# Kernel optimization log

Measured on AMD Instinct MI355X. Metric: run time of the kernel, lower is better.

## Reference

```python
import jax, jax.numpy as jnp
import numpy as np

# Bit-slice quantization config (MSB-first; first 1-bit slice is the sign slice)
INPUT_SLICE = (1, 2, 2, 2)    # 7 bits total
WEIGHT_SLICE = (1, 2, 2, 2)   # 7 bits total
INPUT_GRAN = 32               # input quant granularity along K (per unfolded row)
WEIGHT_GRAN_K = 32            # weight quant granularity along K
WEIGHT_GRAN_N = 32            # weight quant granularity along N
STRIDE = 1
PAD = 1
KSIZE = 3


def _quantize(x, max_abs, total_bits):
    """Symmetric per-granule quantization to signed total_bits integers."""
    max_val = float((1 << (total_bits - 1)) - 1)
    scale = max_abs / max_val
    scale = jnp.where(scale == 0, jnp.ones_like(scale), scale)
    q = jnp.clip(jnp.round(x / scale), -max_val, max_val)
    return q, scale


def _slice_recombine(q, slice_bits):
    """Emulate the bit-slice path: decompose signed int q (two's complement)
    into slices per slice_bits (MSB first), then recombine exactly as the
    crossbar MapReduce accumulation 'sum_i slice_i * 2^offset_i' would."""
    t = int(sum(slice_bits))
    qi = q.astype(jnp.int32)
    u = jnp.where(qi < 0, qi + (1 << t), qi)  # two's complement unsigned rep
    recomb = jnp.zeros_like(u)
    off = t
    for b in slice_bits:  # fixed, small slice loop
        off -= b
        s = (u >> off) & ((1 << b) - 1)
        recomb = recomb + (s << off)
    recomb = jnp.where(recomb >= (1 << (t - 1)), recomb - (1 << t), recomb)
    return recomb.astype(jnp.float32)


def _fake_quant_input(x):
    # x: (B, L, K) unfolded activations; granularity (1, INPUT_GRAN)
    B, L, K = x.shape
    g = INPUT_GRAN
    xg = x.reshape(B, L, K // g, g)
    max_abs = jnp.max(jnp.abs(xg), axis=-1, keepdims=True)
    q, scale = _quantize(xg, max_abs, sum(INPUT_SLICE))
    q = _slice_recombine(q, INPUT_SLICE)
    deq = (q * scale).reshape(B, L, K)
    # straight-through estimator (matches custom autograd conv2d_mem_func)
    return x + jax.lax.stop_gradient(deq - x)


def _fake_quant_weight(w):
    # w: (K, N) reshaped weight; granularity (WEIGHT_GRAN_K, WEIGHT_GRAN_N)
    K, N = w.shape
    gk, gn = WEIGHT_GRAN_K, WEIGHT_GRAN_N
    wg = w.reshape(K // gk, gk, N // gn, gn)
    max_abs = jnp.max(jnp.abs(wg), axis=(1, 3), keepdims=True)
    q, scale = _quantize(wg, max_abs, sum(WEIGHT_SLICE))
    q = _slice_recombine(q, WEIGHT_SLICE)
    deq = (q * scale).reshape(K, N)
    return w + jax.lax.stop_gradient(deq - w)


def _unfold(x, k, stride, pad):
    # torch.F.unfold semantics -> (B, L, C*k*k), C-major ordering
    B, C, H, W = x.shape
    xp = jnp.pad(x, ((0, 0), (0, 0), (pad, pad), (pad, pad)))
    Ho = (H + 2 * pad - k) // stride + 1
    Wo = (W + 2 * pad - k) // stride + 1
    cols = []
    for ki in range(k):  # fixed small kernel loop
        for kj in range(k):
            cols.append(xp[:, :, ki:ki + stride * Ho:stride, kj:kj + stride * Wo:stride])
    patches = jnp.stack(cols, axis=2)              # (B, C, k*k, Ho, Wo)
    patches = patches.reshape(B, C * k * k, Ho * Wo)
    return patches.transpose(0, 2, 1), Ho, Wo      # (B, L, K)


def setup_inputs() -> dict:
    key = jax.random.key(0)
    k1, k2, k3 = jax.random.split(key, 3)
    B, C, H, W = 8, 256, 56, 56
    N = 256
    fan_in = C * KSIZE * KSIZE
    x = jax.random.normal(k1, (B, C, H, W), dtype=jnp.float32)
    weight = jax.random.normal(k2, (N, C, KSIZE, KSIZE), dtype=jnp.float32) / np.sqrt(fan_in)
    bias = jax.random.normal(k3, (N,), dtype=jnp.float32) / np.sqrt(fan_in)
    return {"input": x, "weight": weight, "bias": bias}


def reference(input, weight, bias):
    B = input.shape[0]
    N = weight.shape[0]
    cols, Ho, Wo = _unfold(input, KSIZE, STRIDE, PAD)     # (B, L, K)
    w2d = weight.reshape(N, -1).T                         # (K, N)
    xq = _fake_quant_input(cols)
    wq = _fake_quant_weight(w2d)
    out = jnp.einsum('blk,kn->bln', xq, wq) + bias        # (B, L, N)
    out = out.transpose(0, 2, 1).reshape(B, N, Ho, Wo)    # fold with 1x1 kernel
    return out
```

## Files before the change

### kernel.cpp

```cpp
#include <hip/hip_runtime.h>
#include <hip/hip_bf16.h>
#include <stdint.h>

#define KD 2304
#define LD 3136
#define ND 256
#define MD 25088
#define CD 256
#define PITCH 64
#define PROWS 58
#define PLANE (PROWS * PITCH)

typedef __bf16 bf16x8 __attribute__((ext_vector_type(8)));
typedef float f32x4 __attribute__((ext_vector_type(4)));
typedef float f32x4u __attribute__((ext_vector_type(4), aligned(4)));

__device__ __forceinline__ void gload_lds16(const void* g, void* l) {
  __builtin_amdgcn_global_load_lds(
      (const __attribute__((address_space(1))) unsigned int*)g,
      (__attribute__((address_space(3))) unsigned int*)l, 16, 0, 0);
}

__global__ __launch_bounds__(256) void prep_kernel(
    const float* __restrict__ x, float* __restrict__ xpad,
    const float* __restrict__ w, __hip_bfloat16* __restrict__ wqT) {
  if (blockIdx.x < 2048) {
    const int plane = blockIdx.x;
    const float* src = x + (size_t)plane * LD;
    float* dst = xpad + (size_t)plane * PLANE;
    const int cc4 = (threadIdx.x & 15) * 4;
    const int r0 = threadIdx.x >> 4;
#pragma unroll
    for (int p = 0; p < 4; ++p) {
      const int r = r0 + p * 16;
      if (r >= PROWS) continue;
      f32x4 o = {0.f, 0.f, 0.f, 0.f};
      if (r >= 1 && r <= 56) {
        const float* srow = src + (r - 1) * 56;
        if (cc4 == 0) {
          f32x4u v = *(const f32x4u*)(srow);
          o[1] = v[0]; o[2] = v[1]; o[3] = v[2];
        } else if (cc4 <= 52) {
          o = *(const f32x4u*)(srow + cc4 - 1);
        } else if (cc4 == 56) {
          f32x4u v = *(const f32x4u*)(srow + 52);
          o[0] = v[3];
        }
      }
      *(f32x4*)(dst + r * PITCH + cc4) = o;
    }
  } else {
    const int wb = blockIdx.x - 2048;
    const int gk = wb % 72;
    const int gn = wb / 72;
    const int n = gn * 32 + (threadIdx.x >> 3);
    const int k = gk * 32 + (threadIdx.x & 7) * 4;
    const float4 v = *(const float4*)(w + (size_t)n * KD + k);
    float a = fmaxf(fmaxf(fabsf(v.x), fabsf(v.y)), fmaxf(fabsf(v.z), fabsf(v.w)));
#pragma unroll
    for (int m = 1; m <= 32; m <<= 1) a = fmaxf(a, __shfl_xor(a, m, 64));
    __shared__ float red[4];
    if ((threadIdx.x & 63) == 0) red[threadIdx.x >> 6] = a;
    __syncthreads();
    const float mx = fmaxf(fmaxf(red[0], red[1]), fmaxf(red[2], red[3]));
    const float r63 = (mx == 0.f) ? 0.f : 63.f / mx;
    const float scale = mx * (1.f / 63.f);
    ushort4 o;
    o.x = __builtin_bit_cast(unsigned short, __float2bfloat16(rintf(v.x * r63) * scale));
    o.y = __builtin_bit_cast(unsigned short, __float2bfloat16(rintf(v.y * r63) * scale));
    o.z = __builtin_bit_cast(unsigned short, __float2bfloat16(rintf(v.z * r63) * scale));
    o.w = __builtin_bit_cast(unsigned short, __float2bfloat16(rintf(v.w * r63) * scale));
    *(ushort4*)((unsigned short*)wqT + (size_t)n * KD + k) = o;
  }
}

__device__ __forceinline__ void qload_u(const float* __restrict__ pb, int p0,
                                        int c0, f32x4u (&win)[5][3]) {
#pragma unroll
  for (int dc = 0; dc < 5; ++dc) {
    const int cdc = (c0 + dc > 255) ? 255 : c0 + dc;
    const float* cp = pb + p0 + cdc * PLANE;
#pragma unroll
    for (int di = 0; di < 3; ++di)
      win[dc][di] = *(const f32x4u*)(cp + di * PITCH);
  }
}

template <int KP0>
__device__ __forceinline__ void qfinishT(const f32x4u (&win)[5][3],
                                         char* __restrict__ as_base,
                                         int lane, unsigned cbase) {
  float v[32];
#pragma unroll
  for (int t = 0; t < 32; ++t) {
    const int idx = KP0 + t;
    v[t] = win[idx / 9][(idx % 9) / 3][(idx % 9) % 3];
  }
  float m16[16];
#pragma unroll
  for (int t = 0; t < 16; ++t)
    m16[t] = fmaxf(__builtin_fabsf(v[2 * t]), __builtin_fabsf(v[2 * t + 1]));
#pragma unroll
  for (int t = 0; t < 8; ++t) m16[t] = fmaxf(m16[t], m16[t + 8]);
#pragma unroll
  for (int t = 0; t < 4; ++t) m16[t] = fmaxf(m16[t], m16[t + 4]);
  const float mx = fmaxf(fmaxf(m16[0], m16[1]), fmaxf(m16[2], m16[3]));
  float r63 = 63.f * __builtin_amdgcn_rcpf(mx);
  r63 = (mx == 0.f) ? 0.f : r63;
  const float scale = mx * (1.f / 63.f);
  unsigned pk[16];
#pragma unroll
  for (int t = 0; t < 16; ++t) {
    const float a = rintf(v[2 * t] * r63) * scale;
    const float b = rintf(v[2 * t + 1] * r63) * scale;
    unsigned d;
    asm("v_cvt_pk_bf16_f32 %0, %1, %2" : "=v"(d) : "v"(a), "v"(b));
    pk[t] = d;
  }
  char* row = as_base + lane * 128;
  const unsigned swz = (unsigned)((lane & 7) << 4);
#pragma unroll
  for (int s = 0; s < 4; ++s) {
    uint4 o = {pk[4 * s], pk[4 * s + 1], pk[4 * s + 2], pk[4 * s + 3]};
    *(uint4*)(row + ((cbase + (unsigned)(s * 16)) ^ swz)) = o;
  }
}

#define SW_FIN(PH, DST, CB)                                                   \
  switch (PH) {                                                               \
    case 0: qfinishT<0>(win, DST, lane, CB); break;                           \
    case 1: qfinishT<1>(win, DST, lane, CB); break;                           \
    case 2: qfinishT<2>(win, DST, lane, CB); break;                           \
    case 3: qfinishT<3>(win, DST, lane, CB); break;                           \
    case 4: qfinishT<4>(win, DST, lane, CB); break;                           \
    case 5: qfinishT<5>(win, DST, lane, CB); break;                           \
    case 6: qfinishT<6>(win, DST, lane, CB); break;                           \
    case 7: qfinishT<7>(win, DST, lane, CB); break;                           \
    default: qfinishT<8>(win, DST, lane, CB); break;                          \
  }

__device__ __forceinline__ void stage_ns(const unsigned short* __restrict__ wsrc,
                                         int k0, int lane, int w,
                                         char* __restrict__ NsH) {
#pragma unroll
  for (int sg = 0; sg < 8; ++sg) {
    const int c = w * 8 + sg;
    const int row = c * 8 + (lane >> 3);
    const int u = (lane & 7) ^ (row & 7);
    gload_lds16(wsrc + (size_t)row * KD + k0 + u * 8, NsH + c * 1024 + lane * 16);
  }
}

__device__ __forceinline__ void mfma_phase(
    const char* __restrict__ As0, const char* __restrict__ As1,
    const char* __restrict__ Ns0, const char* __restrict__ Ns1,
    f32x4 (&acc)[4][4], int w, int lq, int hv) {
#pragma unroll
  for (int kk = 0; kk < 4; ++kk) {
    const char* NsH = (kk < 2) ? Ns0 : Ns1;
    const char* AsH = (kk < 2) ? As0 : As1;
    const int kl = kk & 1;
    bf16x8 af[4], bf[4];
#pragma unroll
    for (int i = 0; i < 4; ++i) {
      const unsigned rn = (unsigned)(w * 64 + i * 16 + lq);
      const unsigned u = (unsigned)((kl * 4 + hv) ^ (rn & 7));
      af[i] = *(const bf16x8*)(NsH + rn * 128u + u * 16u);
    }
#pragma unroll
    for (int j = 0; j < 4; ++j) {
      const unsigned rm = (unsigned)(j * 16 + lq);
      const unsigned u = (unsigned)((kl * 4 + hv) ^ (rm & 7));
      bf[j] = *(const bf16x8*)(AsH + rm * 128u + u * 16u);
    }
#pragma unroll
    for (int i = 0; i < 4; ++i)
#pragma unroll
      for (int j = 0; j < 4; ++j)
        acc[i][j] = __builtin_amdgcn_mfma_f32_16x16x32_bf16(
            af[i], bf[j], acc[i][j], 0, 0, 0);
  }
}

__global__ __launch_bounds__(256, 2) void fused_gemm_kernel(
    const float* __restrict__ xpad, const __hip_bfloat16* __restrict__ wqT,
    const float* __restrict__ bias, float* __restrict__ out) {
  extern __shared__ char smem[];
  char* As0 = smem;
  char* As1 = smem + 8192;
  char* Ns0 = smem + 16384;
  char* Ns1 = smem + 49152;
  const int tid = threadIdx.x;
  const int lane = tid & 63;
  const int w = __builtin_amdgcn_readfirstlane(tid >> 6);

  const int bid = blockIdx.x;
  const int mt = (bid & 7) * 49 + (bid >> 3);
  const int m0 = mt * 64;

  const int b = m0 / LD;
  const int l = m0 - b * LD + lane;
  const int i = l / 56;
  const int j = l - i * 56;
  const float* pb = xpad + (size_t)b * CD * PLANE;
  const int p0 = i * PITCH + j;
  const unsigned short* wsrc = (const unsigned short*)wqT;

  char* as_dst = (w < 2) ? As0 : As1;
  const unsigned cb = (unsigned)((w & 1) * 64);
  const int lq = lane & 15, hv = lane >> 4;

  f32x4 acc[4][4] = {};
  f32x4u win[5][3];

  int kq = 32 * w;
  int ph = kq % 9;
  qload_u(pb, p0, kq / 9, win);

  for (int R = 0; R < 18; ++R) {
    stage_ns(wsrc, R * 128, lane, w, Ns0);
    stage_ns(wsrc, R * 128 + 64, lane, w, Ns1);
    __builtin_amdgcn_sched_barrier(0);

    SW_FIN(ph, as_dst, cb);

    kq += 128;
    ph += 2; if (ph >= 9) ph -= 9;
    qload_u(pb, p0, kq / 9, win);

    asm volatile("s_waitcnt vmcnt(15) lgkmcnt(0)\n\ts_barrier" ::: "memory");
    __builtin_amdgcn_sched_barrier(0);

    __builtin_amdgcn_s_setprio(1);
    mfma_phase(As0, As1, Ns0, Ns1, acc, w, lq, hv);
    __builtin_amdgcn_s_setprio(0);

    asm volatile("s_waitcnt lgkmcnt(0)\n\ts_barrier" ::: "memory");
    __builtin_amdgcn_sched_barrier(0);
  }

#pragma unroll
  for (int i4 = 0; i4 < 4; ++i4) {
    const int nb = w * 64 + i4 * 16 + hv * 4;
    const float4 b4 = *(const float4*)&bias[nb];
#pragma unroll
    for (int j4 = 0; j4 < 4; ++j4) {
      const int m = m0 + j4 * 16 + lq;
      const int ll = m - b * LD;
      float* op = out + ((size_t)b * ND + nb) * LD + ll;
      op[0]      = acc[i4][j4].x + b4.x;
      op[LD]     = acc[i4][j4].y + b4.y;
      op[2 * LD] = acc[i4][j4].z + b4.z;
      op[3 * LD] = acc[i4][j4].w + b4.w;
    }
  }
}

extern "C" void kernel_launch(void* const* d_in, const int* in_sizes, int n_in,
                              void* d_out, int out_size, void* d_ws, size_t ws_size,
                              hipStream_t stream) {
  const float* x = (const float*)d_in[0];
  const float* wgt = (const float*)d_in[1];
  const float* bias = (const float*)d_in[2];
  float* out = (float*)d_out;

  float* xpad = (float*)d_ws;
  __hip_bfloat16* wqT = (__hip_bfloat16*)((char*)d_ws + 30408704);

  prep_kernel<<<2048 + 576, 256, 0, stream>>>(x, xpad, wgt, wqT);
  fused_gemm_kernel<<<392, 256, 80 * 1024, stream>>>(xpad, wqT, bias, out);
}
```

Measured before the change: 70.27 us.

## Double GEMM M-tile to 128 with 8 waves per block sharing weight tile

Each block now covers 128 output rows with 512 threads (two M-halves by four N-quarters). Each 256x128 weight K-chunk staged in LDS is shared by both M-halves, halving weight traffic per output. The LDS rows widen to 256 bytes with a 16-way XOR swizzle. In exchange the grid drops to 196 blocks, which may underfill the 256 CUs, and LDS grows to 96KB per block.

```diff
diff --git a/kernel.cpp b/kernel.cpp
--- a/kernel.cpp
+++ b/kernel.cpp
@@ -88,8 +88,8 @@
 
 template <int KP0>
 __device__ __forceinline__ void qfinishT(const f32x4u (&win)[5][3],
-                                         char* __restrict__ as_base,
-                                         int lane, unsigned cbase) {
+                                         char* __restrict__ as_row,
+                                         unsigned swz, unsigned cbase) {
   float v[32];
 #pragma unroll
   for (int t = 0; t < 32; ++t) {
@@ -117,61 +117,56 @@
     asm("v_cvt_pk_bf16_f32 %0, %1, %2" : "=v"(d) : "v"(a), "v"(b));
     pk[t] = d;
   }
-  char* row = as_base + lane * 128;
-  const unsigned swz = (unsigned)((lane & 7) << 4);
 #pragma unroll
   for (int s = 0; s < 4; ++s) {
     uint4 o = {pk[4 * s], pk[4 * s + 1], pk[4 * s + 2], pk[4 * s + 3]};
-    *(uint4*)(row + ((cbase + (unsigned)(s * 16)) ^ swz)) = o;
-  }
-}
-
-#define SW_FIN(PH, DST, CB)                                                   \
+    *(uint4*)(as_row + ((cbase + (unsigned)(s * 16)) ^ swz)) = o;
+  }
+}
+
+#define SW_FIN(PH, ROW, SWZ, CB)                                              \
   switch (PH) {                                                               \
-    case 0: qfinishT<0>(win, DST, lane, CB); break;                           \
-    case 1: qfinishT<1>(win, DST, lane, CB); break;                           \
-    case 2: qfinishT<2>(win, DST, lane, CB); break;                           \
-    case 3: qfinishT<3>(win, DST, lane, CB); break;                           \
-    case 4: qfinishT<4>(win, DST, lane, CB); break;                           \
-    case 5: qfinishT<5>(win, DST, lane, CB); break;                           \
-    case 6: qfinishT<6>(win, DST, lane, CB); break;                           \
-    case 7: qfinishT<7>(win, DST, lane, CB); break;                           \
-    default: qfinishT<8>(win, DST, lane, CB); break;                          \
+    case 0: qfinishT<0>(win, ROW, SWZ, CB); break;                            \
+    case 1: qfinishT<1>(win, ROW, SWZ, CB); break;                            \
+    case 2: qfinishT<2>(win, ROW, SWZ, CB); break;                            \
+    case 3: qfinishT<3>(win, ROW, SWZ, CB); break;                            \
+    case 4: qfinishT<4>(win, ROW, SWZ, CB); break;                            \
+    case 5: qfinishT<5>(win, ROW, SWZ, CB); break;                            \
+    case 6: qfinishT<6>(win, ROW, SWZ, CB); break;                            \
+    case 7: qfinishT<7>(win, ROW, SWZ, CB); break;                            \
+    default: qfinishT<8>(win, ROW, SWZ, CB); break;                           \
   }
 
 __device__ __forceinline__ void stage_ns(const unsigned short* __restrict__ wsrc,
                                          int k0, int lane, int w,
-                                         char* __restrict__ NsH) {
+                                         char* __restrict__ Ns) {
 #pragma unroll
   for (int sg = 0; sg < 8; ++sg) {
     const int c = w * 8 + sg;
-    const int row = c * 8 + (lane >> 3);
-    const int u = (lane & 7) ^ (row & 7);
-    gload_lds16(wsrc + (size_t)row * KD + k0 + u * 8, NsH + c * 1024 + lane * 16);
-  }
-}
-
-__device__ __forceinline__ void mfma_phase(
-    const char* __restrict__ As0, const char* __restrict__ As1,
-    const char* __restrict__ Ns0, const char* __restrict__ Ns1,
-    f32x4 (&acc)[4][4], int w, int lq, int hv) {
+    const int row = c * 4 + (lane >> 4);
+    const int u = (lane & 15) ^ (row & 15);
+    gload_lds16(wsrc + (size_t)row * KD + k0 + u * 8, Ns + c * 1024 + lane * 16);
+  }
+}
+
+__device__ __forceinline__ void mfma_phase(const char* __restrict__ As,
+                                           const char* __restrict__ Ns,
+                                           f32x4 (&acc)[4][4], int wn, int wm,
+                                           int lq, int hv) {
 #pragma unroll
   for (int kk = 0; kk < 4; ++kk) {
-    const char* NsH = (kk < 2) ? Ns0 : Ns1;
-    const char* AsH = (kk < 2) ? As0 : As1;
-    const int kl = kk & 1;
     bf16x8 af[4], bf[4];
 #pragma unroll
     for (int i = 0; i < 4; ++i) {
-      const unsigned rn = (unsigned)(w * 64 + i * 16 + lq);
-      const unsigned u = (unsigned)((kl * 4 + hv) ^ (rn & 7));
-      af[i] = *(const bf16x8*)(NsH + rn * 128u + u * 16u);
+      const unsigned rn = (unsigned)(wn * 64 + i * 16 + lq);
+      const unsigned u = (unsigned)((kk * 4 + hv) ^ (rn & 15));
+      af[i] = *(const bf16x8*)(Ns + rn * 256u + u * 16u);
     }
 #pragma unroll
     for (int j = 0; j < 4; ++j) {
-      const unsigned rm = (unsigned)(j * 16 + lq);
-      const unsigned u = (unsigned)((kl * 4 + hv) ^ (rm & 7));
-      bf[j] = *(const bf16x8*)(AsH + rm * 128u + u * 16u);
+      const unsigned rm = (unsigned)(wm * 64 + j * 16 + lq);
+      const unsigned u = (unsigned)((kk * 4 + hv) ^ (rm & 15));
+      bf[j] = *(const bf16x8*)(As + rm * 256u + u * 16u);
     }
 #pragma unroll
     for (int i = 0; i < 4; ++i)
@@ -182,47 +177,49 @@
   }
 }
 
-__global__ __launch_bounds__(256, 2) void fused_gemm_kernel(
+__global__ __launch_bounds__(512, 2) void fused_gemm_kernel(
     const float* __restrict__ xpad, const __hip_bfloat16* __restrict__ wqT,
     const float* __restrict__ bias, float* __restrict__ out) {
   extern __shared__ char smem[];
-  char* As0 = smem;
-  char* As1 = smem + 8192;
-  char* Ns0 = smem + 16384;
-  char* Ns1 = smem + 49152;
+  char* As = smem;
+  char* Ns = smem + 32768;
   const int tid = threadIdx.x;
   const int lane = tid & 63;
   const int w = __builtin_amdgcn_readfirstlane(tid >> 6);
+  const int wm = w >> 2, ks = w & 3, wn = w & 3;
 
   const int bid = blockIdx.x;
-  const int mt = (bid & 7) * 49 + (bid >> 3);
-  const int m0 = mt * 64;
-
-  const int b = m0 / LD;
-  const int l = m0 - b * LD + lane;
+  const int xcd = bid & 7;
+  const int idx = bid >> 3;
+  const int mt = (xcd < 4) ? (xcd * 25 + idx) : (100 + (xcd - 4) * 24 + idx);
+  const int m0 = mt * 128;
+
+  const int gb = m0 + wm * 64;
+  const int b = gb / LD;
+  const int l = gb - b * LD + lane;
   const int i = l / 56;
   const int j = l - i * 56;
   const float* pb = xpad + (size_t)b * CD * PLANE;
   const int p0 = i * PITCH + j;
+  char* as_row = As + (wm * 64 + lane) * 256;
+  const unsigned swz = (unsigned)((lane & 15) << 4);
+  const unsigned cb = (unsigned)(ks * 64);
   const unsigned short* wsrc = (const unsigned short*)wqT;
 
-  char* as_dst = (w < 2) ? As0 : As1;
-  const unsigned cb = (unsigned)((w & 1) * 64);
   const int lq = lane & 15, hv = lane >> 4;
 
   f32x4 acc[4][4] = {};
   f32x4u win[5][3];
 
-  int kq = 32 * w;
+  int kq = 32 * ks;
   int ph = kq % 9;
   qload_u(pb, p0, kq / 9, win);
 
   for (int R = 0; R < 18; ++R) {
-    stage_ns(wsrc, R * 128, lane, w, Ns0);
-    stage_ns(wsrc, R * 128 + 64, lane, w, Ns1);
+    stage_ns(wsrc, R * 128, lane, w, Ns);
     __builtin_amdgcn_sched_barrier(0);
 
-    SW_FIN(ph, as_dst, cb);
+    SW_FIN(ph, as_row, swz, cb);
 
     kq += 128;
     ph += 2; if (ph >= 9) ph -= 9;
@@ -232,7 +229,7 @@
     __builtin_amdgcn_sched_barrier(0);
 
     __builtin_amdgcn_s_setprio(1);
-    mfma_phase(As0, As1, Ns0, Ns1, acc, w, lq, hv);
+    mfma_phase(As, Ns, acc, wn, wm, lq, hv);
     __builtin_amdgcn_s_setprio(0);
 
     asm volatile("s_waitcnt lgkmcnt(0)\n\ts_barrier" ::: "memory");
@@ -241,11 +238,11 @@
 
 #pragma unroll
   for (int i4 = 0; i4 < 4; ++i4) {
-    const int nb = w * 64 + i4 * 16 + hv * 4;
+    const int nb = wn * 64 + i4 * 16 + hv * 4;
     const float4 b4 = *(const float4*)&bias[nb];
 #pragma unroll
     for (int j4 = 0; j4 < 4; ++j4) {
-      const int m = m0 + j4 * 16 + lq;
+      const int m = m0 + wm * 64 + j4 * 16 + lq;
       const int ll = m - b * LD;
       float* op = out + ((size_t)b * ND + nb) * LD + ll;
       op[0]      = acc[i4][j4].x + b4.x;
@@ -268,5 +265,5 @@
   __hip_bfloat16* wqT = (__hip_bfloat16*)((char*)d_ws + 30408704);
 
   prep_kernel<<<2048 + 576, 256, 0, stream>>>(x, xpad, wgt, wqT);
-  fused_gemm_kernel<<<392, 256, 80 * 1024, stream>>>(xpad, wqT, bias, out);
-}
+  fused_gemm_kernel<<<196, 512, 96 * 1024, stream>>>(xpad, wqT, bias, out);
+}
```

Result: slower. 74.60 us (+6.2%).

## Drop padded input copy; read unpadded input directly with boundary masks

Applied to the files above, without the earlier changes.

Removes the prep pass that wrote a zero-padded copy of the input into workspace. The GEMM now loads 3x3 windows straight from the unpadded input, using clamped addresses, lane shuffles of the loaded vector, and a per-lane boundary mask multiply to supply the zero padding. This saves writing and rereading about 30 MB of padded activations. In exchange, address math in the load path gets more complex and rows lose their 16-byte pitch alignment, so the loads are unaligned and may split across cache lines.

```diff
diff --git a/kernel.cpp b/kernel.cpp
--- a/kernel.cpp
+++ b/kernel.cpp
@@ -7,9 +7,6 @@
 #define ND 256
 #define MD 25088
 #define CD 256
-#define PITCH 64
-#define PROWS 58
-#define PLANE (PROWS * PITCH)
 
 typedef __bf16 bf16x8 __attribute__((ext_vector_type(8)));
 typedef float f32x4 __attribute__((ext_vector_type(4)));
@@ -21,80 +18,63 @@
       (__attribute__((address_space(3))) unsigned int*)l, 16, 0, 0);
 }
 
-__global__ __launch_bounds__(256) void prep_kernel(
-    const float* __restrict__ x, float* __restrict__ xpad,
+__global__ __launch_bounds__(256) void quant_w_kernel(
     const float* __restrict__ w, __hip_bfloat16* __restrict__ wqT) {
-  if (blockIdx.x < 2048) {
-    const int plane = blockIdx.x;
-    const float* src = x + (size_t)plane * LD;
-    float* dst = xpad + (size_t)plane * PLANE;
-    const int cc4 = (threadIdx.x & 15) * 4;
-    const int r0 = threadIdx.x >> 4;
-#pragma unroll
-    for (int p = 0; p < 4; ++p) {
-      const int r = r0 + p * 16;
-      if (r >= PROWS) continue;
-      f32x4 o = {0.f, 0.f, 0.f, 0.f};
-      if (r >= 1 && r <= 56) {
-        const float* srow = src + (r - 1) * 56;
-        if (cc4 == 0) {
-          f32x4u v = *(const f32x4u*)(srow);
-          o[1] = v[0]; o[2] = v[1]; o[3] = v[2];
-        } else if (cc4 <= 52) {
-          o = *(const f32x4u*)(srow + cc4 - 1);
-        } else if (cc4 == 56) {
-          f32x4u v = *(const f32x4u*)(srow + 52);
-          o[0] = v[3];
-        }
-      }
-      *(f32x4*)(dst + r * PITCH + cc4) = o;
-    }
-  } else {
-    const int wb = blockIdx.x - 2048;
-    const int gk = wb % 72;
-    const int gn = wb / 72;
-    const int n = gn * 32 + (threadIdx.x >> 3);
-    const int k = gk * 32 + (threadIdx.x & 7) * 4;
-    const float4 v = *(const float4*)(w + (size_t)n * KD + k);
-    float a = fmaxf(fmaxf(fabsf(v.x), fabsf(v.y)), fmaxf(fabsf(v.z), fabsf(v.w)));
-#pragma unroll
-    for (int m = 1; m <= 32; m <<= 1) a = fmaxf(a, __shfl_xor(a, m, 64));
-    __shared__ float red[4];
-    if ((threadIdx.x & 63) == 0) red[threadIdx.x >> 6] = a;
-    __syncthreads();
-    const float mx = fmaxf(fmaxf(red[0], red[1]), fmaxf(red[2], red[3]));
-    const float r63 = (mx == 0.f) ? 0.f : 63.f / mx;
-    const float scale = mx * (1.f / 63.f);
-    ushort4 o;
-    o.x = __builtin_bit_cast(unsigned short, __float2bfloat16(rintf(v.x * r63) * scale));
-    o.y = __builtin_bit_cast(unsigned short, __float2bfloat16(rintf(v.y * r63) * scale));
-    o.z = __builtin_bit_cast(unsigned short, __float2bfloat16(rintf(v.z * r63) * scale));
-    o.w = __builtin_bit_cast(unsigned short, __float2bfloat16(rintf(v.w * r63) * scale));
-    *(ushort4*)((unsigned short*)wqT + (size_t)n * KD + k) = o;
-  }
-}
-
-__device__ __forceinline__ void qload_u(const float* __restrict__ pb, int p0,
-                                        int c0, f32x4u (&win)[5][3]) {
+  const int gk = blockIdx.x % 72;
+  const int gn = blockIdx.x / 72;
+  const int n = gn * 32 + (threadIdx.x >> 3);
+  const int k = gk * 32 + (threadIdx.x & 7) * 4;
+  const float4 v = *(const float4*)(w + (size_t)n * KD + k);
+  float a = fmaxf(fmaxf(fabsf(v.x), fabsf(v.y)), fmaxf(fabsf(v.z), fabsf(v.w)));
+#pragma unroll
+  for (int m = 1; m <= 32; m <<= 1) a = fmaxf(a, __shfl_xor(a, m, 64));
+  __shared__ float red[4];
+  if ((threadIdx.x & 63) == 0) red[threadIdx.x >> 6] = a;
+  __syncthreads();
+  const float mx = fmaxf(fmaxf(red[0], red[1]), fmaxf(red[2], red[3]));
+  const float r63 = (mx == 0.f) ? 0.f : 63.f / mx;
+  const float scale = mx * (1.f / 63.f);
+  ushort4 o;
+  o.x = __builtin_bit_cast(unsigned short, __float2bfloat16(rintf(v.x * r63) * scale));
+  o.y = __builtin_bit_cast(unsigned short, __float2bfloat16(rintf(v.y * r63) * scale));
+  o.z = __builtin_bit_cast(unsigned short, __float2bfloat16(rintf(v.z * r63) * scale));
+  o.w = __builtin_bit_cast(unsigned short, __float2bfloat16(rintf(v.w * r63) * scale));
+  *(ushort4*)((unsigned short*)wqT + (size_t)n * KD + k) = o;
+}
+
+__device__ __forceinline__ void qload_x(const float* __restrict__ xb,
+                                        const int (&off)[3], int c0,
+                                        f32x4u (&win)[5][3]) {
 #pragma unroll
   for (int dc = 0; dc < 5; ++dc) {
     const int cdc = (c0 + dc > 255) ? 255 : c0 + dc;
-    const float* cp = pb + p0 + cdc * PLANE;
-#pragma unroll
-    for (int di = 0; di < 3; ++di)
-      win[dc][di] = *(const f32x4u*)(cp + di * PITCH);
+    const int cb = cdc * LD;
+#pragma unroll
+    for (int di = 0; di < 3; ++di) {
+      const int ad = cb + off[di];
+      int cl = (ad < 0) ? 0 : ad;
+      cl = (cl > CD * LD - 4) ? (CD * LD - 4) : cl;
+      const int d = ad - cl;
+      f32x4u v = *(const f32x4u*)(xb + cl);
+      if (d < 0)       { v[2] = v[1]; v[1] = v[0]; }
+      else if (d == 1) { v[0] = v[1]; v[1] = v[2]; v[2] = v[3]; }
+      else if (d >= 2) { v[0] = v[2]; v[1] = v[3]; }
+      win[dc][di] = v;
+    }
   }
 }
 
 template <int KP0>
 __device__ __forceinline__ void qfinishT(const f32x4u (&win)[5][3],
+                                         const float (&msk)[3][3],
                                          char* __restrict__ as_base,
                                          int lane, unsigned cbase) {
   float v[32];
 #pragma unroll
   for (int t = 0; t < 32; ++t) {
     const int idx = KP0 + t;
-    v[t] = win[idx / 9][(idx % 9) / 3][(idx % 9) % 3];
+    v[t] = win[idx / 9][(idx % 9) / 3][(idx % 9) % 3] *
+           msk[(idx % 9) / 3][(idx % 9) % 3];
   }
   float m16[16];
 #pragma unroll
@@ -128,15 +108,15 @@
 
 #define SW_FIN(PH, DST, CB)                                                   \
   switch (PH) {                                                               \
-    case 0: qfinishT<0>(win, DST, lane, CB); break;                           \
-    case 1: qfinishT<1>(win, DST, lane, CB); break;                           \
-    case 2: qfinishT<2>(win, DST, lane, CB); break;                           \
-    case 3: qfinishT<3>(win, DST, lane, CB); break;                           \
-    case 4: qfinishT<4>(win, DST, lane, CB); break;                           \
-    case 5: qfinishT<5>(win, DST, lane, CB); break;                           \
-    case 6: qfinishT<6>(win, DST, lane, CB); break;                           \
-    case 7: qfinishT<7>(win, DST, lane, CB); break;                           \
-    default: qfinishT<8>(win, DST, lane, CB); break;                          \
+    case 0: qfinishT<0>(win, msk, DST, lane, CB); break;                      \
+    case 1: qfinishT<1>(win, msk, DST, lane, CB); break;                      \
+    case 2: qfinishT<2>(win, msk, DST, lane, CB); break;                      \
+    case 3: qfinishT<3>(win, msk, DST, lane, CB); break;                      \
+    case 4: qfinishT<4>(win, msk, DST, lane, CB); break;                      \
+    case 5: qfinishT<5>(win, msk, DST, lane, CB); break;                      \
+    case 6: qfinishT<6>(win, msk, DST, lane, CB); break;                      \
+    case 7: qfinishT<7>(win, msk, DST, lane, CB); break;                      \
+    default: qfinishT<8>(win, msk, DST, lane, CB); break;                     \
   }
 
 __device__ __forceinline__ void stage_ns(const unsigned short* __restrict__ wsrc,
@@ -183,7 +163,7 @@
 }
 
 __global__ __launch_bounds__(256, 2) void fused_gemm_kernel(
-    const float* __restrict__ xpad, const __hip_bfloat16* __restrict__ wqT,
+    const float* __restrict__ x, const __hip_bfloat16* __restrict__ wqT,
     const float* __restrict__ bias, float* __restrict__ out) {
   extern __shared__ char smem[];
   char* As0 = smem;
@@ -202,8 +182,13 @@
   const int l = m0 - b * LD + lane;
   const int i = l / 56;
   const int j = l - i * 56;
-  const float* pb = xpad + (size_t)b * CD * PLANE;
-  const int p0 = i * PITCH + j;
+  const float* xb = x + (size_t)b * CD * LD;
+  const int off[3] = {l - 57, l - 1, l + 55};
+  const float rv0 = (i > 0) ? 1.f : 0.f, rv2 = (i < 55) ? 1.f : 0.f;
+  const float cv0 = (j > 0) ? 1.f : 0.f, cv2 = (j < 55) ? 1.f : 0.f;
+  const float msk[3][3] = {{rv0 * cv0, rv0, rv0 * cv2},
+                           {cv0, 1.f, cv2},
+                           {rv2 * cv0, rv2, rv2 * cv2}};
   const unsigned short* wsrc = (const unsigned short*)wqT;
 
   char* as_dst = (w < 2) ? As0 : As1;
@@ -215,7 +200,7 @@
 
   int kq = 32 * w;
   int ph = kq % 9;
-  qload_u(pb, p0, kq / 9, win);
+  qload_x(xb, off, kq / 9, win);
 
   for (int R = 0; R < 18; ++R) {
     stage_ns(wsrc, R * 128, lane, w, Ns0);
@@ -226,7 +211,7 @@
 
     kq += 128;
     ph += 2; if (ph >= 9) ph -= 9;
-    qload_u(pb, p0, kq / 9, win);
+    qload_x(xb, off, kq / 9, win);
 
     asm volatile("s_waitcnt vmcnt(15) lgkmcnt(0)\n\ts_barrier" ::: "memory");
     __builtin_amdgcn_sched_barrier(0);
@@ -264,9 +249,8 @@
   const float* bias = (const float*)d_in[2];
   float* out = (float*)d_out;
 
-  float* xpad = (float*)d_ws;
-  __hip_bfloat16* wqT = (__hip_bfloat16*)((char*)d_ws + 30408704);
-
-  prep_kernel<<<2048 + 576, 256, 0, stream>>>(x, xpad, wgt, wqT);
-  fused_gemm_kernel<<<392, 256, 80 * 1024, stream>>>(xpad, wqT, bias, out);
-}
+  __hip_bfloat16* wqT = (__hip_bfloat16*)d_ws;
+
+  quant_w_kernel<<<576, 256, 0, stream>>>(wgt, wqT);
+  fused_gemm_kernel<<<392, 256, 80 * 1024, stream>>>(x, wqT, bias, out);
+}
```

New measurement: 85.46 us. 21.6% more time.
